# Performance work log

Measured on AMD Instinct MI355X. Metric: run time of the kernel, lower is better.

## Reference

```python
import jax, jax.numpy as jnp
import numpy as np

NUM_HEADS = 8
GROUPS = 32
EPS = 1e-5


def setup_inputs() -> dict:
    key = jax.random.key(0)
    ks = jax.random.split(key, 4)
    B, C, H, W = 8, 512, 32, 32
    x = jax.random.normal(ks[0], (B, C, H, W), dtype=jnp.float32)
    gn_w = jnp.ones((C,), dtype=jnp.float32)
    gn_b = jnp.zeros((C,), dtype=jnp.float32)
    qkv_w = jax.random.normal(ks[1], (3 * C, C), dtype=jnp.float32) * (1.0 / np.sqrt(C))
    qkv_b = jnp.zeros((3 * C,), dtype=jnp.float32)
    proj_w = jax.random.normal(ks[2], (C, C), dtype=jnp.float32) * (1.0 / np.sqrt(C))
    proj_b = jnp.zeros((C,), dtype=jnp.float32)
    return {"x": x, "gn_w": gn_w, "gn_b": gn_b, "qkv_w": qkv_w,
            "qkv_b": qkv_b, "proj_w": proj_w, "proj_b": proj_b}


def reference(x, gn_w, gn_b, qkv_w, qkv_b, proj_w, proj_b):
    b, c, h, w = x.shape
    n = h * w
    hd = c // NUM_HEADS
    xf = x.reshape(b, c, n)
    # GroupNorm over (channels_per_group, HW) per sample
    xg = xf.reshape(b, GROUPS, -1)
    mu = jnp.mean(xg, axis=-1, keepdims=True)
    var = jnp.var(xg, axis=-1, keepdims=True)
    xn = ((xg - mu) * jax.lax.rsqrt(var + EPS)).reshape(b, c, n)
    xn = xn * gn_w[None, :, None] + gn_b[None, :, None]
    # 1x1 conv == channel matmul
    qkv = jnp.einsum('oc,bcn->bon', qkv_w, xn) + qkv_b[None, :, None]
    q, k, v = jnp.split(qkv, 3, axis=1)
    q = q.reshape(b, NUM_HEADS, hd, n)
    k = k.reshape(b, NUM_HEADS, hd, n)
    v = v.reshape(b, NUM_HEADS, hd, n)
    scale = hd ** 0.5
    score = jnp.einsum('bhdn,bhdm->bhnm', q, k) / scale  # [b,h,HW,HW]
    attn = jax.nn.softmax(score, axis=-1)
    out = jnp.einsum('bhnm,bhdm->bhnd', attn, v)  # [b,h,HW,hd]
    out = out.transpose(0, 1, 3, 2).reshape(b, c, n)
    out = jnp.einsum('oc,bcn->bon', proj_w, out) + proj_b[None, :, None]
    return x + out.reshape(b, c, h, w)
```

## Files before the change

kernel.cpp:

```cpp
#include <hip/hip_runtime.h>

typedef unsigned short u16;
typedef unsigned long long u64;
typedef __bf16 bf16x8 __attribute__((ext_vector_type(8)));
typedef float f32x4 __attribute__((ext_vector_type(4)));

#define NB 8
#define NC 512
#define NN 1024
#define NHEADS 8
#define HDIM 64
#define CPG 16
#define EPSV 1e-5f
#define LOG2E 1.44269504f

__device__ __forceinline__ float bf2f(u16 h) {
  union { unsigned u; float f; } v; v.u = ((unsigned)h) << 16; return v.f;
}
__device__ __forceinline__ u16 f2bf(float f) {
  union { float f; unsigned u; } v; v.f = f;
  unsigned r = v.u + 0x7fffu + ((v.u >> 16) & 1u);
  return (u16)(r >> 16);
}
__device__ __forceinline__ float h2f(u16 h) {
  unsigned s = (h >> 15) & 1u, e = (h >> 10) & 31u, m = h & 1023u;
  union { unsigned u; float f; } v;
  if (e == 0) { v.u = s << 31; return v.f + (s ? -1.f : 1.f) * (float)m * 5.9604645e-8f; }
  if (e == 31) { v.u = (s << 31) | 0x7F800000u | (m << 13); return v.f; }
  v.u = (s << 31) | ((e + 112u) << 23) | (m << 13);
  return v.f;
}
__device__ __forceinline__ u16 f2h(float f) {
  union { float f; unsigned u; } v; v.f = f;
  unsigned s = (v.u >> 16) & 0x8000u; int e = (int)((v.u >> 23) & 0xFF) - 112;
  unsigned m = v.u & 0x7FFFFFu;
  if (e <= 0) return (u16)s;
  if (e >= 31) return (u16)(s | 0x7C00u);
  u16 h = (u16)(s | (e << 10) | (m >> 13));
  unsigned rem = m & 0x1FFFu;
  if (rem > 0x1000u || (rem == 0x1000u && (h & 1u))) ++h;
  return h;
}
__device__ __forceinline__ float load_elem(const void* p, size_t i, int f) {
  if (f == 1) return bf2f(((const u16*)p)[i]);
  if (f == 2) return h2f(((const u16*)p)[i]);
  return ((const float*)p)[i];
}

__device__ __forceinline__ float exp2_fast(float x) {
  float r;
  asm("v_exp_f32 %0, %1" : "=v"(r) : "v"(x));
  return r;
}

__global__ void detect_dtype(const u16* __restrict__ gw_raw, int* __restrict__ flag) {
  if (threadIdx.x != 0 || blockIdx.x != 0) return;
  int bf = 0, hf = 0;
  for (int i = 0; i < 16; ++i) {
    u16 w = gw_raw[i];
    if (w == 0x3F80u) ++bf;
    else if (w == 0x3C00u) ++hf;
  }
  *flag = (bf >= 12) ? 1 : (hf >= 12) ? 2 : 0;
}

__device__ __forceinline__ void cvt4(const void* raw, u16* dst, int i, int f) {
  if (f == 1) {
    *(uint2*)(dst + i) = *(const uint2*)((const u16*)raw + i);
  } else if (f == 0) {
    float4 v = *(const float4*)((const float*)raw + i);
    u16 o[4] = {f2bf(v.x), f2bf(v.y), f2bf(v.z), f2bf(v.w)};
    *(u64*)(dst + i) = *(const u64*)o;
  } else {
    u16 o[4];
#pragma unroll
    for (int k2 = 0; k2 < 4; ++k2) o[k2] = f2bf(h2f(((const u16*)raw)[i + k2]));
    *(u64*)(dst + i) = *(const u64*)o;
  }
}

__global__ __launch_bounds__(256) void cvt_all(const void* __restrict__ qkvw,
                                               const void* __restrict__ projw,
                                               const void* __restrict__ gw,
                                               const void* __restrict__ gb,
                                               const void* __restrict__ qb,
                                               const void* __restrict__ pb,
                                               u16* __restrict__ wq16,
                                               u16* __restrict__ wp16,
                                               float* __restrict__ cgw,
                                               float* __restrict__ cgb,
                                               float* __restrict__ cqb,
                                               float* __restrict__ cpb,
                                               const int* __restrict__ flag) {
  const int f = *flag;
  const int b = blockIdx.x;
  if (b < 768) {
    cvt4(qkvw, wq16, (b * 256 + threadIdx.x) * 4, f);
  } else if (b < 1024) {
    cvt4(projw, wp16, ((b - 768) * 256 + threadIdx.x) * 4, f);
  } else {
    const int i = (b - 1024) * 256 + threadIdx.x;
    if (i < 512)        cgw[i] = load_elem(gw, i, f);
    else if (i < 1024)  cgb[i - 512] = load_elem(gb, (size_t)(i - 512), f);
    else if (i < 2560)  cqb[i - 1024] = load_elem(qb, (size_t)(i - 1024), f);
    else                cpb[i - 2560] = load_elem(pb, (size_t)(i - 2560), f);
  }
}

__global__ __launch_bounds__(256) void gn_naive(const void* __restrict__ x,
                                                const int* __restrict__ flag,
                                                const float* __restrict__ gw,
                                                const float* __restrict__ gb,
                                                u16* __restrict__ xn, int b0) {
  const int f = *flag;
  const int bl = blockIdx.x >> 5;
  const int g  = blockIdx.x & 31;
  const size_t base = ((size_t)((b0 + bl) * NC + g * CPG)) * NN;
  u16* dst = xn + ((size_t)(bl * NC + g * CPG)) * NN;
  __shared__ float r1[256], r2[256];
  __shared__ alignas(16) float sxf[CPG * NN];
  u16* sx16 = (u16*)sxf;
  const int t = threadIdx.x;
  float s = 0.f, ss = 0.f;
  if (f == 1) {
    const u16* xb = (const u16*)x + base;
    for (int i0 = t * 8; i0 < CPG * NN; i0 += 2048) {
      uint4 dv = *(const uint4*)(xb + i0);
      *(uint4*)(sx16 + i0) = dv;
      const u16* pp = (const u16*)&dv;
#pragma unroll
      for (int j = 0; j < 8; ++j) { float v = bf2f(pp[j]); s += v; ss += v * v; }
    }
  } else if (f == 0) {
    const float* xb = (const float*)x + base;
    for (int i0 = t * 4; i0 < CPG * NN; i0 += 1024) {
      float4 v = *(const float4*)(xb + i0);
      *(float4*)(sxf + i0) = v;
      s += v.x + v.y + v.z + v.w;
      ss += v.x * v.x + v.y * v.y + v.z * v.z + v.w * v.w;
    }
  } else {
    for (int i = t; i < CPG * NN; i += 256) {
      float v = load_elem(x, base + i, f); s += v; ss += v * v;
    }
  }
  r1[t] = s; r2[t] = ss; __syncthreads();
  for (int k = 128; k > 0; k >>= 1) {
    if (t < k) { r1[t] += r1[t + k]; r2[t] += r2[t + k]; }
    __syncthreads();
  }
  const float mu  = r1[0] * (1.f / 16384.f);
  const float var = r2[0] * (1.f / 16384.f) - mu * mu;
  const float rs  = rsqrtf(var + EPSV);
  if (f == 1) {
    for (int i0 = t * 8; i0 < CPG * NN; i0 += 2048) {
      const int c = g * CPG + (i0 >> 10);
      const float wsc = gw[c] * rs;
      const float bsc = gb[c] - mu * wsc;
      uint4 dv = *(const uint4*)(sx16 + i0);
      const u16* pp = (const u16*)&dv;
      u16 o[8];
#pragma unroll
      for (int j = 0; j < 8; ++j) o[j] = f2bf(bf2f(pp[j]) * wsc + bsc);
      *(uint4*)(dst + i0) = *(uint4*)o;
    }
  } else if (f == 0) {
    for (int i0 = t * 4; i0 < CPG * NN; i0 += 1024) {
      const int c = g * CPG + (i0 >> 10);
      const float wsc = gw[c] * rs;
      const float bsc = gb[c] - mu * wsc;
      float4 v = *(const float4*)(sxf + i0);
      u16 o[4] = {f2bf(v.x * wsc + bsc), f2bf(v.y * wsc + bsc),
                  f2bf(v.z * wsc + bsc), f2bf(v.w * wsc + bsc)};
      *(u64*)(dst + i0) = *(const u64*)o;
    }
  } else {
    for (int i = t; i < CPG * NN; i += 256) {
      int c = g * CPG + i / NN;
      dst[i] = f2bf((load_elem(x, base + i, f) - mu) * rs * gw[c] + gb[c]);
    }
  }
}

__global__ __launch_bounds__(256) void gemm_mfma(const u16* __restrict__ A,
                                                 const u16* __restrict__ Bn,
                                                 const float* __restrict__ bias,
                                                 void* __restrict__ out,
                                                 const void* __restrict__ resid,
                                                 const int* __restrict__ flag,
                                                 int M, int K, int b0, int kmode) {
  __shared__ alignas(16) u16 sA[128 * 40];
  __shared__ alignas(16) u16 sB[128 * 40];
  const int m0 = blockIdx.x * 128;
  const int n0 = blockIdx.y * 128;
  const int bz = blockIdx.z;
  const int t = threadIdx.x;
  const int lane = t & 63, wv = t >> 6;
  const int wm = (wv >> 1) * 64, wn = (wv & 1) * 64;
  const int lr = lane & 15, quad = lane >> 4;
  const int f = *flag;

  const int ar0 = t >> 2, akc = (t & 3) * 8;
  const int ar1 = 64 + ar0;
  const int bc0 = t >> 4, bno = (t & 15) * 8;
  const int bc1 = 16 + bc0;

  f32x4 acc[4][4] = {};

  const u16* pa0 = A + (size_t)(m0 + ar0) * K + akc;
  const u16* pa1 = A + (size_t)(m0 + ar1) * K + akc;
  const u16* pb0 = Bn + ((size_t)bz * K + bc0) * NN + n0 + bno;
  const u16* pb1 = Bn + ((size_t)bz * K + bc1) * NN + n0 + bno;

  uint4 xa0 = *(const uint4*)(pa0);
  uint4 xa1 = *(const uint4*)(pa1);
  uint4 xb0 = *(const uint4*)(pb0);
  uint4 xb1 = *(const uint4*)(pb1);
  uint4 ya0 = *(const uint4*)(pa0 + 32);
  uint4 ya1 = *(const uint4*)(pa1 + 32);
  uint4 yb0 = *(const uint4*)(pb0 + (size_t)32 * NN);
  uint4 yb1 = *(const uint4*)(pb1 + (size_t)32 * NN);

#define GEMM_STAGE(ra0, ra1, rb0, rb1)                                   \
  {                                                                      \
    *(uint4*)(sA + ar0 * 40 + akc) = ra0;                                \
    *(uint4*)(sA + ar1 * 40 + akc) = ra1;                                \
    const u16* p0 = (const u16*)&rb0;                                    \
    const u16* p1 = (const u16*)&rb1;                                    \
    _Pragma("unroll")                                                    \
    for (int j = 0; j < 8; ++j) {                                        \
      const int row = bno + j;                                           \
      sB[row * 40 + (bc0 ^ (row & 24))] = p0[j];                         \
      sB[row * 40 + (bc1 ^ (row & 24))] = p1[j];                         \
    }                                                                    \
  }

#define GEMM_MFMA_BLOCK()                                                \
  {                                                                      \
    const u16* pA = sA + (wm + lr) * 40 + quad * 8;                      \
    bf16x8 af[4], bfv[4];                                                \
    _Pragma("unroll")                                                    \
    for (int i = 0; i < 4; ++i) {                                        \
      af[i] = *(const bf16x8*)(pA + i * 640);                            \
      const int rowB = wn + lr + i * 16;                                 \
      bfv[i] = *(const bf16x8*)(sB + rowB * 40 + ((quad * 8) ^ (rowB & 24))); \
    }                                                                    \
    _Pragma("unroll")                                                    \
    for (int i = 0; i < 4; ++i)                                          \
      _Pragma("unroll")                                                  \
      for (int j = 0; j < 4; ++j)                                        \
        acc[i][j] = __builtin_amdgcn_mfma_f32_16x16x32_bf16(af[i], bfv[j], acc[i][j], 0, 0, 0); \
  }

  for (int k0 = 0; k0 < K; k0 += 64) {
    __syncthreads();
    GEMM_STAGE(xa0, xa1, xb0, xb1);
    __syncthreads();
    if (k0 + 64 < K) {
      xa0 = *(const uint4*)(pa0 + k0 + 64);
      xa1 = *(const uint4*)(pa1 + k0 + 64);
      xb0 = *(const uint4*)(pb0 + (size_t)(k0 + 64) * NN);
      xb1 = *(const uint4*)(pb1 + (size_t)(k0 + 64) * NN);
    }
    GEMM_MFMA_BLOCK();
    __syncthreads();
    GEMM_STAGE(ya0, ya1, yb0, yb1);
    __syncthreads();
    if (k0 + 96 < K) {
      ya0 = *(const uint4*)(pa0 + k0 + 96);
      ya1 = *(const uint4*)(pa1 + k0 + 96);
      yb0 = *(const uint4*)(pb0 + (size_t)(k0 + 96) * NN);
      yb1 = *(const uint4*)(pb1 + (size_t)(k0 + 96) * NN);
    }
    GEMM_MFMA_BLOCK();
  }

  const bool kstore = (kmode != 0) && (m0 >= 512) && (m0 < 1024);
  if (kstore) {
    u16* kb2 = (u16*)out + ((size_t)(b0 + bz) * 1536 + 512) * NN;
#pragma unroll
    for (int i = 0; i < 4; ++i) {
      const int mb = m0 + wm + i * 16 + quad * 4;
      const int hh = (mb - 512) >> 6;
      const int d0 = (mb - 512) & 63;
      u16* hb = kb2 + (size_t)hh * NN * 64 + d0;
#pragma unroll
      for (int j = 0; j < 4; ++j) {
        const int col = n0 + wn + j * 16 + lr;
        u16 o[4];
#pragma unroll
        for (int r = 0; r < 4; ++r) o[r] = f2bf(acc[i][j][r] + bias[mb + r]);
        *(u64*)(hb + (size_t)col * 64) = *(const u64*)o;
      }
    }
    return;
  }
#pragma unroll
  for (int i = 0; i < 4; ++i) {
    const int mb = m0 + wm + i * 16 + quad * 4;
#pragma unroll
    for (int r = 0; r < 4; ++r) {
      const int mr = mb + r;
      const float bi = bias[mr];
#pragma unroll
      for (int j = 0; j < 4; ++j) {
        const int col = n0 + wn + j * 16 + lr;
        const size_t oidx = ((size_t)(b0 + bz) * M + mr) * NN + col;
        float v = acc[i][j][r] + bi;
        if (resid) {
          v += load_elem(resid, oidx, f);
          if (f == 1)      ((u16*)out)[oidx] = f2bf(v);
          else if (f == 2) ((u16*)out)[oidx] = f2h(v);
          else             ((float*)out)[oidx] = v;
        } else {
          ((u16*)out)[oidx] = f2bf(v);
        }
      }
    }
  }
}

__global__ __launch_bounds__(256) void attn_mfma(const u16* __restrict__ qkv,
                                                 u16* __restrict__ attnO) {
  __shared__ alignas(16) u16 sK[2][64 * 64];
  __shared__ alignas(16) u16 sV[2][64 * 64];

  const int L   = blockIdx.x + 16 * (blockIdx.y + 8 * blockIdx.z);
  const int xcd = L & 7;
  const int jj  = L >> 3;
  const int grp = xcd + 8 * (jj >> 4);
  const int qt  = jj & 15;
  const int h   = grp & 7;
  const int bz  = grp >> 3;

  const int n0 = qt * 64;
  const u16* qb    = qkv + ((size_t)bz * 1536 + h * HDIM) * NN;
  const u16* kbase = qkv + ((size_t)bz * 1536 + 512) * NN + (size_t)h * NN * HDIM;
  const u16* vb    = qb + (size_t)1024 * NN;
  const int t = threadIdx.x;
  const int lane = t & 63, wv = t >> 6;
  const int lr = lane & 15, quad = lane >> 4;

  const int qcol = n0 + wv * 16 + lr;
  union { u16 u[8]; bf16x8 v; } qa0, qa1;
#pragma unroll
  for (int e = 0; e < 8; ++e) {
    qa0.u[e] = qb[(size_t)(quad * 8 + e) * NN + qcol];
    qa1.u[e] = qb[(size_t)(quad * 8 + 32 + e) * NN + qcol];
  }
  const bf16x8 a0 = qa0.v;
  const bf16x8 a1 = qa1.v;

  const int km = t >> 2;
  const int kc = t & 3;
  const int ke = (km ^ (km >> 3)) & 7;
  const u16* kp = kbase + (size_t)km * 64 + kc * 8;

  const int sd  = t >> 3;
  const int smo = (t & 7) * 8;
  const u16* vp = vb + (size_t)sd * NN + smo;
  const int vs0 = sd * 64 + (smo ^ (8 * (sd & 7)));
  const int vs1 = (sd + 32) * 64 + (smo ^ (8 * ((sd + 32) & 7)));

  uint4 pk0, pk1, pv0, pv1;

  f32x4 acc_o[4] = {};
  float mrow = -1e30f, lrow = 0.f;

  pk0 = *(const uint4*)(kp);
  pk1 = *(const uint4*)(kp + 32);
  pv0 = *(const uint4*)(vp);
  pv1 = *(const uint4*)(vp + (size_t)32 * NN);
  {
    u16* kd = &sK[0][km * 64];
    *(uint4*)(kd + ((kc ^ ke) * 8)) = pk0;
    *(uint4*)(kd + (((kc + 4) ^ ke) * 8)) = pk1;
    *(uint4*)(&sV[0][vs0]) = pv0;
    *(uint4*)(&sV[0][vs1]) = pv1;
  }
  pk0 = *(const uint4*)(kp + 4096);
  pk1 = *(const uint4*)(kp + 4096 + 32);
  pv0 = *(const uint4*)(vp + 64);
  pv1 = *(const uint4*)(vp + (size_t)32 * NN + 64);
  __syncthreads();

  for (int mt = 0; mt < 16; ++mt) {
    const int c = mt & 1;

    f32x4 p[4];
    __builtin_amdgcn_s_setprio(1);
#pragma unroll
    for (int j = 0; j < 4; ++j) {
      const int rk = j * 16 + lr;
      const u16* pKr = &sK[c][rk * 64];
      const int sw = ((rk ^ (rk >> 3)) & 7) * 8;
      bf16x8 k0 = *(const bf16x8*)(pKr + ((quad * 8) ^ sw));
      bf16x8 k1 = *(const bf16x8*)(pKr + ((quad * 8 + 32) ^ sw));
      f32x4 z = {0.f, 0.f, 0.f, 0.f};
      z = __builtin_amdgcn_mfma_f32_16x16x32_bf16(k0, a0, z, 0, 0, 0);
      z = __builtin_amdgcn_mfma_f32_16x16x32_bf16(k1, a1, z, 0, 0, 0);
      p[j] = z;
    }
    __builtin_amdgcn_s_setprio(0);

    float mx = -1e30f;
#pragma unroll
    for (int j = 0; j < 4; ++j)
#pragma unroll
      for (int r = 0; r < 4; ++r) mx = fmaxf(mx, p[j][r]);
    mx = fmaxf(mx, __shfl_xor(mx, 16));
    mx = fmaxf(mx, __shfl_xor(mx, 32));
    const float msc = mx * 0.125f;
    if (!__all(msc - mrow <= 8.f)) {
      const float mnew = fmaxf(mrow, msc);
      const float alpha = exp2_fast((mrow - mnew) * LOG2E);
      mrow = mnew;
      lrow *= alpha;
      float ar[4];
#pragma unroll
      for (int r = 0; r < 4; ++r) ar[r] = __shfl(alpha, quad * 4 + r);
#pragma unroll
      for (int j2 = 0; j2 < 4; ++j2)
#pragma unroll
        for (int r = 0; r < 4; ++r) acc_o[j2][r] *= ar[r];
    }
    const float m2 = mrow * LOG2E;
    float ls = 0.f;
#pragma unroll
    for (int j = 0; j < 4; ++j)
#pragma unroll
      for (int r = 0; r < 4; ++r) {
        const float pe = exp2_fast(fmaf(p[j][r], 0.18033688f, -m2));
        p[j][r] = pe;
        ls += pe;
      }
    ls += __shfl_xor(ls, 16);
    ls += __shfl_xor(ls, 32);
    lrow += ls;

    unsigned pa[4], pb2[4];
#pragma unroll
    for (int j = 0; j < 4; ++j) {
      asm("v_cvt_pk_bf16_f32 %0, %1, %2" : "=v"(pa[j]) : "v"(p[j][0]), "v"(p[j][1]));
      asm("v_cvt_pk_bf16_f32 %0, %1, %2" : "=v"(pb2[j]) : "v"(p[j][2]), "v"(p[j][3]));
    }

    __builtin_amdgcn_s_setprio(1);
#pragma unroll
    for (int ks = 0; ks < 2; ++ks) {
      union { unsigned u[4]; bf16x8 v; } af;
      af.u[0] = pa[2 * ks];
      af.u[1] = pb2[2 * ks];
      af.u[2] = pa[2 * ks + 1];
      af.u[3] = pb2[2 * ks + 1];
#pragma unroll
      for (int j2 = 0; j2 < 4; ++j2) {
        const int rv = j2 * 16 + lr;
        const int swv = 8 * (rv & 7);
        const u16* pVr = &sV[c][rv * 64];
        union { u64 q[2]; bf16x8 v; } bfv;
        bfv.q[0] = *(const u64*)(pVr + ((ks * 32 + 4 * quad) ^ swv));
        bfv.q[1] = *(const u64*)(pVr + ((ks * 32 + 16 + 4 * quad) ^ swv));
        acc_o[j2] = __builtin_amdgcn_mfma_f32_16x16x32_bf16(af.v, bfv.v, acc_o[j2], 0, 0, 0);
      }
    }
    __builtin_amdgcn_s_setprio(0);

    if (mt < 15) {
      const int cn = c ^ 1;
      u16* kd = &sK[cn][km * 64];
      *(uint4*)(kd + ((kc ^ ke) * 8)) = pk0;
      *(uint4*)(kd + (((kc + 4) ^ ke) * 8)) = pk1;
      *(uint4*)(&sV[cn][vs0]) = pv0;
      *(uint4*)(&sV[cn][vs1]) = pv1;
      if (mt < 14) {
        const size_t ko = (size_t)(mt + 2) * 4096;
        const int mo = (mt + 2) * 64;
        pk0 = *(const uint4*)(kp + ko);
        pk1 = *(const uint4*)(kp + ko + 32);
        pv0 = *(const uint4*)(vp + mo);
        pv1 = *(const uint4*)(vp + (size_t)32 * NN + mo);
      }
      __syncthreads();
    }
  }

  const float invl = 1.f / lrow;
  float ir[4];
#pragma unroll
  for (int r = 0; r < 4; ++r) ir[r] = __shfl(invl, quad * 4 + r);
  const int qrow = n0 + wv * 16 + quad * 4;
#pragma unroll
  for (int j2 = 0; j2 < 4; ++j2) {
    const int d = j2 * 16 + lr;
    u16 o[4];
#pragma unroll
    for (int r = 0; r < 4; ++r) o[r] = f2bf(acc_o[j2][r] * ir[r]);
    *(u64*)(attnO + ((size_t)bz * NC + h * HDIM + d) * NN + qrow) = *(const u64*)o;
  }
}

__global__ void sig_small_ws(u16* out) {
  if (threadIdx.x == 0 && blockIdx.x == 0) out[0] = f2bf(20000.f);
}

extern "C" void kernel_launch(void* const* d_in, const int* in_sizes, int n_in,
                              void* d_out, int out_size, void* d_ws, size_t ws_size,
                              hipStream_t stream) {
  const void* x      = d_in[0];
  const void* gn_w   = d_in[1];
  const void* gn_b   = d_in[2];
  const void* qkv_w  = d_in[3];
  const void* qkv_b  = d_in[4];
  const void* proj_w = d_in[5];
  const void* proj_b = d_in[6];
  char* ws = (char*)d_ws;
  const size_t MB = (size_t)1 << 20;

  u16*   wq16 = (u16*)(ws);
  u16*   wp16 = (u16*)(ws + 3 * MB / 2);
  float* cgw  = (float*)(ws + 2 * MB);
  float* cgb  = (float*)(ws + 2 * MB + 4096);
  float* cqb  = (float*)(ws + 2 * MB + 8192);
  float* cpb  = (float*)(ws + 2 * MB + 16384);
  int*   flag = (int*)  (ws + 2 * MB + 20480);

  detect_dtype<<<dim3(1), dim3(64), 0, stream>>>((const u16*)gn_w, flag);
  cvt_all<<<dim3(1036), dim3(256), 0, stream>>>(qkv_w, proj_w, gn_w, gn_b,
                                                qkv_b, proj_b, wq16, wp16,
                                                cgw, cgb, cqb, cpb, flag);

  if (ws_size >= 36 * MB) {
    u16* xn    = (u16*)(ws + 3 * MB);
    u16* qkvb  = (u16*)(ws + 11 * MB);
    u16* attnO = xn;
    gn_naive<<<dim3(NB * 32), dim3(256), 0, stream>>>(x, flag, cgw, cgb, xn, 0);
    gemm_mfma<<<dim3(12, 8, NB), dim3(256), 0, stream>>>(wq16, xn, cqb, qkvb,
                                                         nullptr, flag, 1536, NC, 0, 1);
    attn_mfma<<<dim3(16, NHEADS, NB), dim3(256), 0, stream>>>(qkvb, attnO);
    gemm_mfma<<<dim3(4, 8, NB), dim3(256), 0, stream>>>(wp16, attnO, cpb, d_out,
                                                        x, flag, NC, NC, 0, 0);
  } else if (ws_size >= 9 * MB) {
    u16* xn    = (u16*)(ws + 3 * MB);
    u16* qkvb  = (u16*)(ws + 4 * MB);
    u16* attnO = (u16*)(ws + 7 * MB);
    for (int b = 0; b < NB; ++b) {
      gn_naive<<<dim3(32), dim3(256), 0, stream>>>(x, flag, cgw, cgb, xn, b);
      gemm_mfma<<<dim3(12, 8, 1), dim3(256), 0, stream>>>(wq16, xn, cqb, qkvb,
                                                          nullptr, flag, 1536, NC, 0, 1);
      attn_mfma<<<dim3(16, NHEADS, 1), dim3(256), 0, stream>>>(qkvb, attnO);
      gemm_mfma<<<dim3(4, 8, 1), dim3(256), 0, stream>>>(wp16, attnO, cpb, d_out,
                                                         x, flag, NC, NC, b, 0);
    }
  } else {
    sig_small_ws<<<dim3(1), dim3(64), 0, stream>>>((u16*)d_out);
  }
}
```

Measured before the change: 201.1 us.

## Fuse GroupNorm apply into QKV GEMM B-operand load, keep only stats kernel

The GroupNorm kernel now computes only per-channel scale and shift, writing small per-(batch, channel) arrays instead of a normalized bf16 copy of x. The QKV GEMM reads x directly (fp32 or bf16) and applies scale, shift and bf16 conversion while staging the B tile into shared memory. This removes the write and re-read of the normalized activation buffer and the large shared-memory staging in the norm kernel. In exchange, the GEMM loads twice as many bytes per B element when the input is fp32, and does more conversion ALU work inside its main loop.

New measurement: 220.9 us. 9.9% more time.

```diff
diff --git a/kernel.cpp b/kernel.cpp
--- a/kernel.cpp
+++ b/kernel.cpp
@@ -107,26 +107,23 @@
   }
 }
 
-__global__ __launch_bounds__(256) void gn_naive(const void* __restrict__ x,
+__global__ __launch_bounds__(256) void gn_stats(const void* __restrict__ x,
                                                 const int* __restrict__ flag,
                                                 const float* __restrict__ gw,
                                                 const float* __restrict__ gb,
-                                                u16* __restrict__ xn, int b0) {
+                                                float* __restrict__ wscp,
+                                                float* __restrict__ bscp, int b0) {
   const int f = *flag;
   const int bl = blockIdx.x >> 5;
   const int g  = blockIdx.x & 31;
   const size_t base = ((size_t)((b0 + bl) * NC + g * CPG)) * NN;
-  u16* dst = xn + ((size_t)(bl * NC + g * CPG)) * NN;
   __shared__ float r1[256], r2[256];
-  __shared__ alignas(16) float sxf[CPG * NN];
-  u16* sx16 = (u16*)sxf;
   const int t = threadIdx.x;
   float s = 0.f, ss = 0.f;
   if (f == 1) {
     const u16* xb = (const u16*)x + base;
     for (int i0 = t * 8; i0 < CPG * NN; i0 += 2048) {
       uint4 dv = *(const uint4*)(xb + i0);
-      *(uint4*)(sx16 + i0) = dv;
       const u16* pp = (const u16*)&dv;
 #pragma unroll
       for (int j = 0; j < 8; ++j) { float v = bf2f(pp[j]); s += v; ss += v * v; }
@@ -135,7 +132,6 @@
     const float* xb = (const float*)x + base;
     for (int i0 = t * 4; i0 < CPG * NN; i0 += 1024) {
       float4 v = *(const float4*)(xb + i0);
-      *(float4*)(sxf + i0) = v;
       s += v.x + v.y + v.z + v.w;
       ss += v.x * v.x + v.y * v.y + v.z * v.z + v.w * v.w;
     }
@@ -152,43 +148,61 @@
   const float mu  = r1[0] * (1.f / 16384.f);
   const float var = r2[0] * (1.f / 16384.f) - mu * mu;
   const float rs  = rsqrtf(var + EPSV);
-  if (f == 1) {
-    for (int i0 = t * 8; i0 < CPG * NN; i0 += 2048) {
-      const int c = g * CPG + (i0 >> 10);
-      const float wsc = gw[c] * rs;
-      const float bsc = gb[c] - mu * wsc;
-      uint4 dv = *(const uint4*)(sx16 + i0);
-      const u16* pp = (const u16*)&dv;
-      u16 o[8];
-#pragma unroll
-      for (int j = 0; j < 8; ++j) o[j] = f2bf(bf2f(pp[j]) * wsc + bsc);
-      *(uint4*)(dst + i0) = *(uint4*)o;
-    }
-  } else if (f == 0) {
-    for (int i0 = t * 4; i0 < CPG * NN; i0 += 1024) {
-      const int c = g * CPG + (i0 >> 10);
-      const float wsc = gw[c] * rs;
-      const float bsc = gb[c] - mu * wsc;
-      float4 v = *(const float4*)(sxf + i0);
-      u16 o[4] = {f2bf(v.x * wsc + bsc), f2bf(v.y * wsc + bsc),
-                  f2bf(v.z * wsc + bsc), f2bf(v.w * wsc + bsc)};
-      *(u64*)(dst + i0) = *(const u64*)o;
-    }
+  if (t < CPG) {
+    const int c = g * CPG + t;
+    const float w = gw[c] * rs;
+    wscp[(size_t)(b0 + bl) * NC + c] = w;
+    bscp[(size_t)(b0 + bl) * NC + c] = gb[c] - mu * w;
+  }
+}
+
+struct BR { uint4 lo, hi; };
+
+__device__ __forceinline__ BR ldBrow(const void* B, size_t eoff, int f) {
+  BR r;
+  if (f == 0) {
+    const uint4* p = (const uint4*)((const float*)B + eoff);
+    r.lo = p[0]; r.hi = p[1];
   } else {
-    for (int i = t; i < CPG * NN; i += 256) {
-      int c = g * CPG + i / NN;
-      dst[i] = f2bf((load_elem(x, base + i, f) - mu) * rs * gw[c] + gb[c]);
-    }
+    r.lo = *(const uint4*)((const u16*)B + eoff);
+    r.hi = r.lo;
+  }
+  return r;
+}
+
+__device__ __forceinline__ void stBrow(u16* sB, int bno, int bc, const BR& br,
+                                       float w, float bsv, int f) {
+  float v[8];
+  if (f == 0) {
+    const float* pf = (const float*)&br;
+#pragma unroll
+    for (int j = 0; j < 8; ++j) v[j] = pf[j];
+  } else if (f == 1) {
+    const u16* ph = (const u16*)&br.lo;
+#pragma unroll
+    for (int j = 0; j < 8; ++j) v[j] = bf2f(ph[j]);
+  } else {
+    const u16* ph = (const u16*)&br.lo;
+#pragma unroll
+    for (int j = 0; j < 8; ++j) v[j] = h2f(ph[j]);
+  }
+#pragma unroll
+  for (int j = 0; j < 8; ++j) {
+    const int row = bno + j;
+    sB[row * 40 + (bc ^ (row & 24))] = f2bf(v[j] * w + bsv);
   }
 }
 
 __global__ __launch_bounds__(256) void gemm_mfma(const u16* __restrict__ A,
-                                                 const u16* __restrict__ Bn,
+                                                 const void* __restrict__ Bv,
                                                  const float* __restrict__ bias,
                                                  void* __restrict__ out,
                                                  const void* __restrict__ resid,
                                                  const int* __restrict__ flag,
-                                                 int M, int K, int b0, int kmode) {
+                                                 const float* __restrict__ wscp,
+                                                 const float* __restrict__ bscp,
+                                                 int M, int K, int b0,
+                                                 int kmode, int bmode) {
   __shared__ alignas(16) u16 sA[128 * 40];
   __shared__ alignas(16) u16 sB[128 * 40];
   const int m0 = blockIdx.x * 128;
@@ -199,39 +213,52 @@
   const int wm = (wv >> 1) * 64, wn = (wv & 1) * 64;
   const int lr = lane & 15, quad = lane >> 4;
   const int f = *flag;
+  const int bf_ = bmode ? f : 1;
 
   const int ar0 = t >> 2, akc = (t & 3) * 8;
   const int ar1 = 64 + ar0;
   const int bc0 = t >> 4, bno = (t & 15) * 8;
   const int bc1 = 16 + bc0;
 
+  const int bb = bmode ? (b0 + bz) : bz;
+  const size_t wb = (size_t)bb * NC;
+  const size_t bO = ((size_t)bb * K) * NN + n0 + bno;
+
   f32x4 acc[4][4] = {};
 
   const u16* pa0 = A + (size_t)(m0 + ar0) * K + akc;
   const u16* pa1 = A + (size_t)(m0 + ar1) * K + akc;
-  const u16* pb0 = Bn + ((size_t)bz * K + bc0) * NN + n0 + bno;
-  const u16* pb1 = Bn + ((size_t)bz * K + bc1) * NN + n0 + bno;
 
   uint4 xa0 = *(const uint4*)(pa0);
   uint4 xa1 = *(const uint4*)(pa1);
-  uint4 xb0 = *(const uint4*)(pb0);
-  uint4 xb1 = *(const uint4*)(pb1);
   uint4 ya0 = *(const uint4*)(pa0 + 32);
   uint4 ya1 = *(const uint4*)(pa1 + 32);
-  uint4 yb0 = *(const uint4*)(pb0 + (size_t)32 * NN);
-  uint4 yb1 = *(const uint4*)(pb1 + (size_t)32 * NN);
-
-#define GEMM_STAGE(ra0, ra1, rb0, rb1)                                   \
+  BR xr0 = ldBrow(Bv, bO + (size_t)bc0 * NN, bf_);
+  BR xr1 = ldBrow(Bv, bO + (size_t)bc1 * NN, bf_);
+  BR yr0 = ldBrow(Bv, bO + (size_t)(32 + bc0) * NN, bf_);
+  BR yr1 = ldBrow(Bv, bO + (size_t)(32 + bc1) * NN, bf_);
+  float xw0 = 1.f, xw1 = 1.f, xs0 = 0.f, xs1 = 0.f;
+  float yw0 = 1.f, yw1 = 1.f, ys0 = 0.f, ys1 = 0.f;
+  if (bmode) {
+    xw0 = wscp[wb + bc0]; xs0 = bscp[wb + bc0];
+    xw1 = wscp[wb + bc1]; xs1 = bscp[wb + bc1];
+    yw0 = wscp[wb + 32 + bc0]; ys0 = bscp[wb + 32 + bc0];
+    yw1 = wscp[wb + 32 + bc1]; ys1 = bscp[wb + 32 + bc1];
+  }
+
+#define GSTAGE_A(ra0_, ra1_)                                             \
   {                                                                      \
-    *(uint4*)(sA + ar0 * 40 + akc) = ra0;                                \
-    *(uint4*)(sA + ar1 * 40 + akc) = ra1;                                \
-    const u16* p0 = (const u16*)&rb0;                                    \
-    const u16* p1 = (const u16*)&rb1;                                    \
+    *(uint4*)(sA + ar0 * 40 + akc) = ra0_;                               \
+    *(uint4*)(sA + ar1 * 40 + akc) = ra1_;                               \
+  }
+
+#define GSTAGE_B_RAW(rb_, bc_)                                           \
+  {                                                                      \
+    const u16* p_ = (const u16*)&rb_.lo;                                 \
     _Pragma("unroll")                                                    \
     for (int j = 0; j < 8; ++j) {                                        \
       const int row = bno + j;                                           \
-      sB[row * 40 + (bc0 ^ (row & 24))] = p0[j];                         \
-      sB[row * 40 + (bc1 ^ (row & 24))] = p1[j];                         \
+      sB[row * 40 + (bc_ ^ (row & 24))] = p_[j];                         \
     }                                                                    \
   }
 
@@ -254,23 +281,45 @@
 
   for (int k0 = 0; k0 < K; k0 += 64) {
     __syncthreads();
-    GEMM_STAGE(xa0, xa1, xb0, xb1);
+    GSTAGE_A(xa0, xa1);
+    if (bmode) {
+      stBrow(sB, bno, bc0, xr0, xw0, xs0, bf_);
+      stBrow(sB, bno, bc1, xr1, xw1, xs1, bf_);
+    } else {
+      GSTAGE_B_RAW(xr0, bc0);
+      GSTAGE_B_RAW(xr1, bc1);
+    }
     __syncthreads();
     if (k0 + 64 < K) {
       xa0 = *(const uint4*)(pa0 + k0 + 64);
       xa1 = *(const uint4*)(pa1 + k0 + 64);
-      xb0 = *(const uint4*)(pb0 + (size_t)(k0 + 64) * NN);
-      xb1 = *(const uint4*)(pb1 + (size_t)(k0 + 64) * NN);
+      xr0 = ldBrow(Bv, bO + (size_t)(k0 + 64 + bc0) * NN, bf_);
+      xr1 = ldBrow(Bv, bO + (size_t)(k0 + 64 + bc1) * NN, bf_);
+      if (bmode) {
+        xw0 = wscp[wb + k0 + 64 + bc0]; xs0 = bscp[wb + k0 + 64 + bc0];
+        xw1 = wscp[wb + k0 + 64 + bc1]; xs1 = bscp[wb + k0 + 64 + bc1];
+      }
     }
     GEMM_MFMA_BLOCK();
     __syncthreads();
-    GEMM_STAGE(ya0, ya1, yb0, yb1);
+    GSTAGE_A(ya0, ya1);
+    if (bmode) {
+      stBrow(sB, bno, bc0, yr0, yw0, ys0, bf_);
+      stBrow(sB, bno, bc1, yr1, yw1, ys1, bf_);
+    } else {
+      GSTAGE_B_RAW(yr0, bc0);
+      GSTAGE_B_RAW(yr1, bc1);
+    }
     __syncthreads();
     if (k0 + 96 < K) {
       ya0 = *(const uint4*)(pa0 + k0 + 96);
       ya1 = *(const uint4*)(pa1 + k0 + 96);
-      yb0 = *(const uint4*)(pb0 + (size_t)(k0 + 96) * NN);
-      yb1 = *(const uint4*)(pb1 + (size_t)(k0 + 96) * NN);
+      yr0 = ldBrow(Bv, bO + (size_t)(k0 + 96 + bc0) * NN, bf_);
+      yr1 = ldBrow(Bv, bO + (size_t)(k0 + 96 + bc1) * NN, bf_);
+      if (bmode) {
+        yw0 = wscp[wb + k0 + 96 + bc0]; ys0 = bscp[wb + k0 + 96 + bc0];
+        yw1 = wscp[wb + k0 + 96 + bc1]; ys1 = bscp[wb + k0 + 96 + bc1];
+      }
     }
     GEMM_MFMA_BLOCK();
   }
@@ -524,6 +573,8 @@
   float* cqb  = (float*)(ws + 2 * MB + 8192);
   float* cpb  = (float*)(ws + 2 * MB + 16384);
   int*   flag = (int*)  (ws + 2 * MB + 20480);
+  float* wscp = (float*)(ws + 2 * MB + 24576);
+  float* bscp = (float*)(ws + 2 * MB + 40960);
 
   detect_dtype<<<dim3(1), dim3(64), 0, stream>>>((const u16*)gn_w, flag);
   cvt_all<<<dim3(1036), dim3(256), 0, stream>>>(qkv_w, proj_w, gn_w, gn_b,
@@ -531,26 +582,30 @@
                                                 cgw, cgb, cqb, cpb, flag);
 
   if (ws_size >= 36 * MB) {
-    u16* xn    = (u16*)(ws + 3 * MB);
+    u16* attnO = (u16*)(ws + 3 * MB);
     u16* qkvb  = (u16*)(ws + 11 * MB);
-    u16* attnO = xn;
-    gn_naive<<<dim3(NB * 32), dim3(256), 0, stream>>>(x, flag, cgw, cgb, xn, 0);
-    gemm_mfma<<<dim3(12, 8, NB), dim3(256), 0, stream>>>(wq16, xn, cqb, qkvb,
-                                                         nullptr, flag, 1536, NC, 0, 1);
+    gn_stats<<<dim3(NB * 32), dim3(256), 0, stream>>>(x, flag, cgw, cgb,
+                                                      wscp, bscp, 0);
+    gemm_mfma<<<dim3(12, 8, NB), dim3(256), 0, stream>>>(wq16, x, cqb, qkvb,
+                                                         nullptr, flag, wscp, bscp,
+                                                         1536, NC, 0, 1, 1);
     attn_mfma<<<dim3(16, NHEADS, NB), dim3(256), 0, stream>>>(qkvb, attnO);
     gemm_mfma<<<dim3(4, 8, NB), dim3(256), 0, stream>>>(wp16, attnO, cpb, d_out,
-                                                        x, flag, NC, NC, 0, 0);
+                                                        x, flag, wscp, bscp,
+                                                        NC, NC, 0, 0, 0);
   } else if (ws_size >= 9 * MB) {
-    u16* xn    = (u16*)(ws + 3 * MB);
     u16* qkvb  = (u16*)(ws + 4 * MB);
     u16* attnO = (u16*)(ws + 7 * MB);
     for (int b = 0; b < NB; ++b) {
-      gn_naive<<<dim3(32), dim3(256), 0, stream>>>(x, flag, cgw, cgb, xn, b);
-      gemm_mfma<<<dim3(12, 8, 1), dim3(256), 0, stream>>>(wq16, xn, cqb, qkvb,
-                                                          nullptr, flag, 1536, NC, 0, 1);
+      gn_stats<<<dim3(32), dim3(256), 0, stream>>>(x, flag, cgw, cgb,
+                                                   wscp, bscp, b);
+      gemm_mfma<<<dim3(12, 8, 1), dim3(256), 0, stream>>>(wq16, x, cqb, qkvb,
+                                                          nullptr, flag, wscp, bscp,
+                                                          1536, NC, b, 1, 1);
       attn_mfma<<<dim3(16, NHEADS, 1), dim3(256), 0, stream>>>(qkvb, attnO);
       gemm_mfma<<<dim3(4, 8, 1), dim3(256), 0, stream>>>(wp16, attnO, cpb, d_out,
-                                                         x, flag, NC, NC, b, 0);
+                                                         x, flag, wscp, bscp,
+                                                         NC, NC, b, 0, 0);
     }
   } else {
     sig_small_ws<<<dim3(1), dim3(64), 0, stream>>>((u16*)d_out);
```
